# Kernel tuning notes

Measured on AMD Instinct MI355X. Metric: run time of the kernel, lower is better.

Reference implementation:

```python
import jax, jax.numpy as jnp
import numpy as np

N = 100000
E = 400000
G = 2000  # number of graphs in batch
IN_DIM = 32
H = 192
L = 4
EPS = 1e-5


def setup_inputs() -> dict:
    key = jax.random.key(0)
    ks = jax.random.split(key, 20)
    x = jax.random.normal(ks[0], (N, IN_DIM), jnp.float32)
    edge_src = jax.random.randint(ks[1], (E,), 0, N, jnp.int32)
    edge_dst = jax.random.randint(ks[2], (E,), 0, N, jnp.int32)
    batch = jnp.sort(jax.random.randint(ks[3], (N,), 0, G, jnp.int32))
    s_in = 1.0 / np.sqrt(IN_DIM)
    s_h = 1.0 / np.sqrt(H)
    return {
        "x": x,
        "edge_src": edge_src,
        "edge_dst": edge_dst,
        "batch": batch,
        # layer 0 (in_dim -> H); weights stored [in, out]
        "Wrel0": jax.random.uniform(ks[4], (IN_DIM, H), jnp.float32, -s_in, s_in),
        "brel0": jax.random.uniform(ks[5], (H,), jnp.float32, -s_in, s_in),
        "Wroot0": jax.random.uniform(ks[6], (IN_DIM, H), jnp.float32, -s_in, s_in),
        # layers 1..3 stacked (H -> H)
        "Wrel": jax.random.uniform(ks[7], (L - 1, H, H), jnp.float32, -s_h, s_h),
        "brel": jax.random.uniform(ks[8], (L - 1, H), jnp.float32, -s_h, s_h),
        "Wroot": jax.random.uniform(ks[9], (L - 1, H, H), jnp.float32, -s_h, s_h),
        # batchnorm affine params for all 4 layers
        "gamma": jnp.ones((L, H), jnp.float32),
        "beta": jnp.zeros((L, H), jnp.float32),
        # head MLP and output
        "Wh1": jax.random.uniform(ks[10], (H, H), jnp.float32, -s_h, s_h),
        "bh1": jax.random.uniform(ks[11], (H,), jnp.float32, -s_h, s_h),
        "Wh2": jax.random.uniform(ks[12], (H, H), jnp.float32, -s_h, s_h),
        "bh2": jax.random.uniform(ks[13], (H,), jnp.float32, -s_h, s_h),
        "Wout": jax.random.uniform(ks[14], (H, 1), jnp.float32, -s_h, s_h),
        "bout": jax.random.uniform(ks[15], (1,), jnp.float32, -s_h, s_h),
    }


def _rel_conv(x, edge_src, edge_dst, Wrel, brel, Wroot):
    # message: lin_rel(x_j); applying the linear at node level first is the
    # same math as per-edge (linear commutes with gather) and cheaper.
    h = x @ Wrel + brel                      # [N, out]
    agg = jax.ops.segment_sum(h[edge_src], edge_dst, num_segments=N)
    return agg + x @ Wroot


def _bn_relu(h, g, b):
    # BatchNorm1d in training mode: batch stats over node dim, biased var
    mu = h.mean(axis=0)
    var = jnp.var(h, axis=0)
    h = (h - mu) * jax.lax.rsqrt(var + EPS) * g + b
    return jax.nn.relu(h)


def reference(x, edge_src, edge_dst, batch, Wrel0, brel0, Wroot0,
              Wrel, brel, Wroot, gamma, beta, Wh1, bh1, Wh2, bh2, Wout, bout):
    h = _bn_relu(_rel_conv(x, edge_src, edge_dst, Wrel0, brel0, Wroot0),
                 gamma[0], beta[0])
    for i in range(L - 1):
        h = _bn_relu(_rel_conv(h, edge_src, edge_dst, Wrel[i], brel[i], Wroot[i]),
                     gamma[i + 1], beta[i + 1])
    # global mean pool over graphs
    sums = jax.ops.segment_sum(h, batch, num_segments=G)          # [G, H]
    cnt = jax.ops.segment_sum(jnp.ones((N,), h.dtype), batch, num_segments=G)
    g = sums / jnp.maximum(cnt, 1.0)[:, None]
    # head MLP (dropout is identity at eval) + output linear
    g = jax.nn.relu(g @ Wh1 + bh1) @ Wh2 + bh2
    return g @ Wout + bout                                        # [G, 1]
```

## Files before the change

### kernel.cpp

```cpp
#include <hip/hip_runtime.h>

#define HDIM 192
#define EPS 1e-5f

typedef __attribute__((ext_vector_type(8))) _Float16 half8;
typedef __attribute__((ext_vector_type(4))) float floatx4;

__device__ __forceinline__ float h2f(ushort u) {
    union { ushort u; _Float16 h; } c; c.u = u; return (float)c.h;
}
__device__ __forceinline__ ushort f2h(float x) {
    _Float16 h = (_Float16)x;
    union { _Float16 h; ushort u; } c; c.h = h; return c.u;
}
__device__ __forceinline__ uint4 pack8(const ushort* h) {
    uint4 p;
    p.x = h[0] | ((uint)h[1] << 16); p.y = h[2] | ((uint)h[3] << 16);
    p.z = h[4] | ((uint)h[5] << 16); p.w = h[6] | ((uint)h[7] << 16);
    return p;
}

__device__ __forceinline__ void gload_lds16(const ushort* g, ushort* l) {
    __builtin_amdgcn_global_load_lds(
        (const __attribute__((address_space(1))) unsigned int*)g,
        (__attribute__((address_space(3))) unsigned int*)l, 16, 0, 0);
}

#define WAITV0() asm volatile("s_waitcnt vmcnt(0)" ::: "memory")


struct PrepArgs {
    const float* src[6];
    ushort*      dst[6];
    int K[6];
    int off[7];
};

__global__ __launch_bounds__(256) void prep_all_k(PrepArgs a)
{
    int idx = blockIdx.x * 256 + threadIdx.x;
    if (idx >= a.off[6]) return;
    int i = 0;
    #pragma unroll
    for (int t = 1; t < 6; ++t) if (idx >= a.off[t]) i = t;
    int r = idx - a.off[i];
    int K = a.K[i];
    int perMat = (K >> 5) * 12 * 64;
    int mat = r / perMat;
    r -= mat * perMat;
    int lane = r & 63;
    int ct = (r >> 6) % 12;
    int kc = r / (12 * 64);
    int col = ct * 16 + (lane & 15);
    int kb  = kc * 32 + (lane >> 4) * 8;
    const float* Wm = a.src[i] + (size_t)mat * K * HDIM;
    ushort* base = a.dst[i] + (size_t)mat * K * HDIM;
    size_t o = (size_t)kc * 6144 + (size_t)(ct * 64 + lane) * 8;
    #pragma unroll
    for (int j = 0; j < 8; ++j)
        base[o + j] = f2h(Wm[(size_t)(kb + j) * HDIM + col]);
}

__global__ __launch_bounds__(256) void conv_half_k(
    const float* __restrict__ src, ushort* __restrict__ dst, int R, int C)
{
    int OC = C >> 3;
    int idx = blockIdx.x * 256 + threadIdx.x;
    if (idx >= R * OC) return;
    int r = idx / OC;
    int o = idx - r * OC;
    float4 v0 = ((const float4*)(src + (size_t)r * C + o * 8))[0];
    float4 v1 = ((const float4*)(src + (size_t)r * C + o * 8))[1];
    float v[8] = {v0.x, v0.y, v0.z, v0.w, v1.x, v1.y, v1.z, v1.w};
    ushort h[8];
    #pragma unroll
    for (int t = 0; t < 8; ++t) h[t] = f2h(v[t]);
    *(uint4*)(dst + (size_t)r * C + o * 8) = pack8(h);
}

template<bool DUAL, bool RELU, bool DEG, bool STATS, int NKC>
__global__ __launch_bounds__(256, 3) void gemm_mfma_k(
    const ushort* __restrict__ A1h, const ushort* __restrict__ W1f,
    const ushort* __restrict__ A2h, const ushort* __restrict__ W2f,
    const float* __restrict__ degf, const float* __restrict__ bias,
    ushort* __restrict__ C, float* __restrict__ pstats, int N, int K)
{
    constexpr int KR   = NKC * 32;
    constexpr int RS   = KR + 8;
    constexpr int SLAB = 64 * RS;
    constexpr int NINSTR = SLAB / 512;
    constexpr int NCH  = DUAL ? 2 * NKC : NKC;
    constexpr int SMEMU = ((DUAL ? 2 * SLAB : SLAB) > 12800)
                            ? (DUAL ? 2 * SLAB : SLAB) : 12800;

    __shared__ float sstat[2][HDIM];
    __shared__ __align__(16) ushort smem[SMEMU];
    const int tid  = threadIdx.x;
    const int wave = tid >> 6;
    const int lane = tid & 63;
    const int row0 = blockIdx.x * 64;
    const int m16 = lane & 15;
    const int g4  = lane >> 4;

    if (STATS && tid < HDIM) { sstat[0][tid] = 0.f; sstat[1][tid] = 0.f; }

    auto stage = [&](const ushort* Ab, int slabOff) {
        #pragma unroll
        for (int i = wave; i < NINSTR; i += 4) {
            int slotB = i * 1024 + lane * 16;
            int r   = slotB / (RS * 2);
            int off = slotB - r * (RS * 2);
            if (off >= KR * 2) off = KR * 2 - 16;
            int rr = row0 + r; if (rr >= N) rr = N - 1;
            gload_lds16(Ab + (size_t)rr * KR + (off >> 1),
                        smem + slabOff + i * 512);
        }
    };

    stage(A1h, 0);
    if constexpr (DUAL) stage(A2h, SLAB);
    WAITV0();
    __builtin_amdgcn_s_barrier();
    __builtin_amdgcn_sched_barrier(0);

    auto loadB = [&](int c, half8* b) {
        bool ph = DUAL && (c >= NKC);
        int kc = ph ? c - NKC : c;
        const ushort* Bp = (ph ? W2f : W1f) + (size_t)kc * 6144
                         + (size_t)(wave * 192 + lane) * 8;
        #pragma unroll
        for (int ct = 0; ct < 3; ++ct)
            b[ct] = *(const half8*)(Bp + ct * 512);
    };

    floatx4 acc[4][3];
    #pragma unroll
    for (int s = 0; s < 4; ++s)
        #pragma unroll
        for (int ct = 0; ct < 3; ++ct) acc[s][ct] = (floatx4){0.f, 0.f, 0.f, 0.f};

    half8 bA[3], bB[3];
    loadB(0, bA);
    #pragma unroll
    for (int c = 0; c < NCH; ++c) {
        if (c + 1 < NCH) loadB(c + 1, (c & 1) ? bA : bB);
        const int base = (DUAL && c >= NKC) ? SLAB : 0;
        const int kc   = (DUAL && c >= NKC) ? c - NKC : c;
        const ushort* aB = smem + base + m16 * RS + kc * 32 + g4 * 8;
        half8 a[4];
        #pragma unroll
        for (int s = 0; s < 4; ++s)
            a[s] = *(const half8*)(aB + s * 16 * RS);
        const half8* bu = (c & 1) ? bB : bA;
        #pragma unroll
        for (int ct = 0; ct < 3; ++ct)
            #pragma unroll
            for (int s = 0; s < 4; ++s)
                acc[s][ct] = __builtin_amdgcn_mfma_f32_16x16x32_f16(a[s], bu[ct], acc[s][ct], 0, 0, 0);
    }

    __syncthreads();
    #pragma unroll
    for (int ct = 0; ct < 3; ++ct) {
        int col = wave * 48 + ct * 16 + m16;
        float bv = bias ? bias[col] : 0.f;
        float lsum = 0.f, lsq = 0.f;
        #pragma unroll
        for (int s = 0; s < 4; ++s) {
            #pragma unroll
            for (int reg = 0; reg < 4; ++reg) {
                int rloc = s * 16 + g4 * 4 + reg;
                int rr = row0 + rloc;
                int rrc = rr < N ? rr : N - 1;
                float v = acc[s][ct][reg] + (DEG ? degf[rrc] * bv : bv);
                if (STATS && rr < N) { lsum += v; lsq += v * v; }
                if (RELU) v = fmaxf(v, 0.f);
                smem[rloc * 200 + col] = f2h(v);
            }
        }
        if (STATS) {
            lsum += __shfl_xor(lsum, 16); lsum += __shfl_xor(lsum, 32);
            lsq  += __shfl_xor(lsq, 16);  lsq  += __shfl_xor(lsq, 32);
            if (g4 == 0) {
                atomicAdd(&sstat[0][col], lsum);
                atomicAdd(&sstat[1][col], lsq);
            }
        }
    }
    __syncthreads();
    {
        int rowsLeft = N - row0; if (rowsLeft > 64) rowsLeft = 64;
        int lim = rowsLeft * 24;
        ushort* Cb = C + (size_t)row0 * HDIM;
        #pragma unroll
        for (int k = 0; k < 6; ++k) {
            int u = tid + k * 256;
            if (u < lim) {
                int r  = u / 24;
                int c8 = (u - r * 24) * 8;
                *(uint4*)(Cb + (size_t)u * 8) =
                    *(const uint4*)(smem + r * 200 + c8);
            }
        }
    }
    if (STATS) {
        if (tid < HDIM) {
            float* pb = pstats + (size_t)blockIdx.x * (2 * HDIM);
            pb[tid]        = sstat[0][tid];
            pb[HDIM + tid] = sstat[1][tid];
        }
    }
}

__global__ __launch_bounds__(256, 3) void gemm_fused_k(
    const ushort* __restrict__ Hraw, const ushort* __restrict__ W1f,
    const ushort* __restrict__ W2f,
    const float* __restrict__ degf, const float* __restrict__ bias,
    const float* __restrict__ instats, const float* __restrict__ gammaL,
    const float* __restrict__ betaL, float invN,
    const int* __restrict__ row_ptr, const int* __restrict__ col,
    ushort* __restrict__ C, float* __restrict__ pstats, int N)
{
    constexpr int KR   = 192;
    constexpr int RS   = 200;
    constexpr int SLAB = 64 * RS;
    constexpr int NINSTR = SLAB / 512;
    constexpr int NKC  = 6, NCH = 12;

    __shared__ float sstat[2][HDIM];
    __shared__ __align__(16) ushort smem[2 * SLAB];
    const int tid  = threadIdx.x;
    const int wave = tid >> 6;
    const int lane = tid & 63;
    const int row0 = blockIdx.x * 64;
    const int m16 = lane & 15;
    const int g4  = lane >> 4;

    #pragma unroll
    for (int i = wave; i < NINSTR; i += 4) {
        int slotB = i * 1024 + lane * 16;
        int r   = slotB / (RS * 2);
        int off = slotB - r * (RS * 2);
        if (off >= KR * 2) off = KR * 2 - 16;
        int rr = row0 + r; if (rr >= N) rr = N - 1;
        gload_lds16(Hraw + (size_t)rr * KR + (off >> 1),
                    smem + SLAB + i * 512);
    }
    WAITV0();
    __builtin_amdgcn_s_barrier();
    __builtin_amdgcn_sched_barrier(0);

    if (tid < HDIM) {
        float mu  = instats[tid] * invN;
        float var = instats[HDIM + tid] * invN - mu * mu;
        float s = gammaL[tid] * rsqrtf(var + EPS);
        sstat[0][tid] = s;
        sstat[1][tid] = betaL[tid] - mu * s;
    }
    __syncthreads();

    const int r = tid >> 2, q = tid & 3;
    {
        ushort* rowp = smem + SLAB + r * RS + q * 48;
        #pragma unroll
        for (int k = 0; k < 6; ++k) {
            uint4 hv = *(uint4*)(rowp + k * 8);
            uint hu[4] = {hv.x, hv.y, hv.z, hv.w};
            ushort oh[8];
            #pragma unroll
            for (int e = 0; e < 4; ++e) {
                int ch = q * 48 + k * 8 + e * 2;
                float v0 = h2f((ushort)(hu[e] & 0xffffu)) * sstat[0][ch]     + sstat[1][ch];
                float v1 = h2f((ushort)(hu[e] >> 16))     * sstat[0][ch + 1] + sstat[1][ch + 1];
                oh[2*e]   = f2h(fmaxf(v0, 0.f));
                oh[2*e+1] = f2h(fmaxf(v1, 0.f));
            }
            *(uint4*)(rowp + k * 8) = pack8(oh);
        }
    }
    {
        float acc[48];
        #pragma unroll
        for (int i = 0; i < 48; ++i) acc[i] = 0.f;
        int rr = row0 + r;
        if (rr < N) {
            int j0 = row_ptr[rr], j1 = row_ptr[rr + 1];
            const ushort* hp = Hraw + q * 48;
            for (int j = j0; j < j1; ++j) {
                int s = col[j];
                const ushort* rp = hp + (size_t)s * KR;
                #pragma unroll
                for (int ck = 0; ck < 6; ++ck) {
                    uint4 hv = *(const uint4*)(rp + ck * 8);
                    uint hu[4] = {hv.x, hv.y, hv.z, hv.w};
                    #pragma unroll
                    for (int e = 0; e < 4; ++e) {
                        int ch = q * 48 + ck * 8 + e * 2;
                        float v0 = h2f((ushort)(hu[e] & 0xffffu)) * sstat[0][ch]     + sstat[1][ch];
                        float v1 = h2f((ushort)(hu[e] >> 16))     * sstat[0][ch + 1] + sstat[1][ch + 1];
                        acc[ck*8 + e*2]     += fmaxf(v0, 0.f);
                        acc[ck*8 + e*2 + 1] += fmaxf(v1, 0.f);
                    }
                }
            }
        }
        ushort* dst = smem + r * RS + q * 48;
        #pragma unroll
        for (int ck = 0; ck < 6; ++ck) {
            ushort oh[8];
            #pragma unroll
            for (int e = 0; e < 8; ++e) oh[e] = f2h(acc[ck*8 + e]);
            *(uint4*)(dst + ck * 8) = pack8(oh);
        }
    }
    __syncthreads();
    if (tid < HDIM) { sstat[0][tid] = 0.f; sstat[1][tid] = 0.f; }

    auto loadB = [&](int c, half8* b) {
        bool ph = (c >= NKC);
        int kc = ph ? c - NKC : c;
        const ushort* Bp = (ph ? W2f : W1f) + (size_t)kc * 6144
                         + (size_t)(wave * 192 + lane) * 8;
        #pragma unroll
        for (int ct = 0; ct < 3; ++ct)
            b[ct] = *(const half8*)(Bp + ct * 512);
    };

    floatx4 acc[4][3];
    #pragma unroll
    for (int s = 0; s < 4; ++s)
        #pragma unroll
        for (int ct = 0; ct < 3; ++ct) acc[s][ct] = (floatx4){0.f, 0.f, 0.f, 0.f};

    half8 bA[3], bB[3];
    loadB(0, bA);
    #pragma unroll
    for (int c = 0; c < NCH; ++c) {
        if (c + 1 < NCH) loadB(c + 1, (c & 1) ? bA : bB);
        const int base = (c >= NKC) ? SLAB : 0;
        const int kc   = (c >= NKC) ? c - NKC : c;
        const ushort* aB = smem + base + m16 * RS + kc * 32 + g4 * 8;
        half8 a[4];
        #pragma unroll
        for (int s = 0; s < 4; ++s)
            a[s] = *(const half8*)(aB + s * 16 * RS);
        const half8* bu = (c & 1) ? bB : bA;
        #pragma unroll
        for (int ct = 0; ct < 3; ++ct)
            #pragma unroll
            for (int s = 0; s < 4; ++s)
                acc[s][ct] = __builtin_amdgcn_mfma_f32_16x16x32_f16(a[s], bu[ct], acc[s][ct], 0, 0, 0);
    }

    __syncthreads();
    #pragma unroll
    for (int ct = 0; ct < 3; ++ct) {
        int colc = wave * 48 + ct * 16 + m16;
        float bv = bias[colc];
        float lsum = 0.f, lsq = 0.f;
        #pragma unroll
        for (int s = 0; s < 4; ++s) {
            #pragma unroll
            for (int reg = 0; reg < 4; ++reg) {
                int rloc = s * 16 + g4 * 4 + reg;
                int rr = row0 + rloc;
                int rrc = rr < N ? rr : N - 1;
                float v = acc[s][ct][reg] + degf[rrc] * bv;
                if (rr < N) { lsum += v; lsq += v * v; }
                smem[rloc * 200 + colc] = f2h(v);
            }
        }
        lsum += __shfl_xor(lsum, 16); lsum += __shfl_xor(lsum, 32);
        lsq  += __shfl_xor(lsq, 16);  lsq  += __shfl_xor(lsq, 32);
        if (g4 == 0) {
            atomicAdd(&sstat[0][colc], lsum);
            atomicAdd(&sstat[1][colc], lsq);
        }
    }
    __syncthreads();
    {
        int rowsLeft = N - row0; if (rowsLeft > 64) rowsLeft = 64;
        int lim = rowsLeft * 24;
        ushort* Cb = C + (size_t)row0 * HDIM;
        #pragma unroll
        for (int k = 0; k < 6; ++k) {
            int u = tid + k * 256;
            if (u < lim) {
                int rr = u / 24;
                int c8 = (u - rr * 24) * 8;
                *(uint4*)(Cb + (size_t)u * 8) =
                    *(const uint4*)(smem + rr * 200 + c8);
            }
        }
    }
    if (tid < HDIM) {
        float* pb = pstats + (size_t)blockIdx.x * (2 * HDIM);
        pb[tid]        = sstat[0][tid];
        pb[HDIM + tid] = sstat[1][tid];
    }
}

__global__ __launch_bounds__(256) void bn_reduce_k(
    const float* __restrict__ pbuf, float* __restrict__ stats, int nb)
{
    __shared__ float red[32][9];
    int t  = threadIdx.x;
    int cl = t & 7;
    int s  = t >> 3;
    int c  = blockIdx.x * 8 + cl;
    float acc = 0.f;
    int b = s;
    for (; b + 96 < nb; b += 128) {
        float a0 = pbuf[(size_t)b * 384 + c];
        float a1 = pbuf[(size_t)(b + 32) * 384 + c];
        float a2 = pbuf[(size_t)(b + 64) * 384 + c];
        float a3 = pbuf[(size_t)(b + 96) * 384 + c];
        acc += a0 + a1 + a2 + a3;
    }
    for (; b < nb; b += 32)
        acc += pbuf[(size_t)b * 384 + c];
    red[s][cl] = acc;
    __syncthreads();
    if (t < 8) {
        float a = 0.f;
        #pragma unroll
        for (int i = 0; i < 32; ++i) a += red[i][t];
        stats[blockIdx.x * 8 + t] = a;
    }
}

__global__ __launch_bounds__(256) void hist_k(
    const int* __restrict__ dst, int* __restrict__ deg, int E)
{
    int e = blockIdx.x * 256 + threadIdx.x;
    if (e < E) atomicAdd(&deg[dst[e]], 1);
}

__global__ __launch_bounds__(256) void block_sum_k(
    const int* __restrict__ deg, int* __restrict__ bsum, int N)
{
    __shared__ int s[256];
    int t = threadIdx.x;
    int n = blockIdx.x * 256 + t;
    s[t] = (n < N) ? deg[n] : 0;
    __syncthreads();
    for (int off = 128; off > 0; off >>= 1) {
        if (t < off) s[t] += s[t + off];
        __syncthreads();
    }
    if (t == 0) bsum[blockIdx.x] = s[0];
}

__global__ __launch_bounds__(512) void scan_bsum_k(int* __restrict__ bsum, int nb)
{
    __shared__ int s[512];
    int t = threadIdx.x;
    int v = (t < nb) ? bsum[t] : 0;
    s[t] = v;
    __syncthreads();
    for (int off = 1; off < 512; off <<= 1) {
        int u = (t >= off) ? s[t - off] : 0;
        __syncthreads();
        s[t] += u;
        __syncthreads();
    }
    if (t < nb) bsum[t] = s[t] - v;
}

__global__ __launch_bounds__(256) void row_ptr_k(
    const int* __restrict__ deg, const int* __restrict__ bsum,
    int* __restrict__ row_ptr, int* __restrict__ cursor,
    float* __restrict__ degf, int N, int E)
{
    __shared__ int s[256];
    int t = threadIdx.x;
    int n = blockIdx.x * 256 + t;
    int v = (n < N) ? deg[n] : 0;
    s[t] = v;
    __syncthreads();
    for (int off = 1; off < 256; off <<= 1) {
        int u = (t >= off) ? s[t - off] : 0;
        __syncthreads();
        s[t] += u;
        __syncthreads();
    }
    int ex = s[t] - v + bsum[blockIdx.x];
    if (n < N) {
        row_ptr[n] = ex;
        cursor[n]  = ex;
        degf[n]    = (float)v;
    }
    if (blockIdx.x == 0 && t == 0) row_ptr[N] = E;
}

__global__ __launch_bounds__(256) void fill_k(
    const int* __restrict__ src, const int* __restrict__ dst,
    int* __restrict__ cursor, int* __restrict__ col, int E)
{
    int e = blockIdx.x * 256 + threadIdx.x;
    if (e < E) {
        int p = atomicAdd(&cursor[dst[e]], 1);
        col[p] = src[e];
    }
}

__global__ __launch_bounds__(256) void gather_h_k(
    const ushort* __restrict__ xh, const int* __restrict__ row_ptr,
    const int* __restrict__ col, ushort* __restrict__ gh, int N, int K)
{
    int OC = K >> 3;
    int idx = blockIdx.x * 256 + threadIdx.x;
    if (idx >= N * OC) return;
    int n = idx / OC;
    int o = idx - n * OC;
    const ushort* hp = xh + o * 8;
    int j0 = row_ptr[n], j1 = row_ptr[n + 1];
    float acc[8] = {0.f,0.f,0.f,0.f,0.f,0.f,0.f,0.f};
    auto addrow = [&](uint4 hv) {
        uint hu[4] = {hv.x, hv.y, hv.z, hv.w};
        #pragma unroll
        for (int t = 0; t < 4; ++t) {
            acc[2*t]   += h2f((ushort)(hu[t] & 0xffffu));
            acc[2*t+1] += h2f((ushort)(hu[t] >> 16));
        }
    };
    int j = j0;
    for (; j + 3 < j1; j += 4) {
        int s0 = col[j], s1 = col[j+1], s2 = col[j+2], s3 = col[j+3];
        uint4 v0 = *(const uint4*)(hp + (size_t)s0 * K);
        uint4 v1 = *(const uint4*)(hp + (size_t)s1 * K);
        uint4 v2 = *(const uint4*)(hp + (size_t)s2 * K);
        uint4 v3 = *(const uint4*)(hp + (size_t)s3 * K);
        addrow(v0); addrow(v1); addrow(v2); addrow(v3);
    }
    for (; j < j1; ++j)
        addrow(*(const uint4*)(hp + (size_t)col[j] * K));
    ushort oh[8];
    #pragma unroll
    for (int t = 0; t < 8; ++t) oh[t] = f2h(acc[t]);
    *(uint4*)(gh + (size_t)n * K + o * 8) = pack8(oh);
}

__global__ __launch_bounds__(192) void pool_bn_k(
    const ushort* __restrict__ h, const float* __restrict__ stats,
    const float* __restrict__ gamma, const float* __restrict__ beta,
    float invN, const int* __restrict__ batch,
    ushort* __restrict__ gsh, int G, int N)
{
    __shared__ int bounds[2];
    int g = blockIdx.x;
    int c = threadIdx.x;
    if (c < 2) {
        int key = g + c;
        int lo = 0, hi = N;
        while (lo < hi) {
            int mid = (lo + hi) >> 1;
            if (batch[mid] < key) lo = mid + 1; else hi = mid;
        }
        bounds[c] = lo;
    }
    __syncthreads();
    int r0 = bounds[0], r1 = bounds[1];
    float mu  = stats[c] * invN;
    float var = stats[HDIM + c] * invN - mu * mu;
    float sc  = gamma[c] * rsqrtf(var + EPS);
    float sh  = beta[c] - mu * sc;
    const ushort* base = h + c;
    float s = 0.f;
    for (int r = r0; r < r1; ++r)
        s += fmaxf(h2f(base[(size_t)r * HDIM]) * sc + sh, 0.f);
    float m = s / fmaxf((float)(r1 - r0), 1.f);
    gsh[(size_t)g * HDIM + c] = f2h(m);
}

__global__ __launch_bounds__(64) void out_dot_k(
    const ushort* __restrict__ g2h, const float* __restrict__ Wout,
    const float* __restrict__ bout, float* __restrict__ out, int G)
{
    int gi = blockIdx.x;
    int t = threadIdx.x;
    float s = 0.f;
    #pragma unroll
    for (int j = 0; j < 3; ++j) {
        int c = t + j * 64;
        s += h2f(g2h[(size_t)gi * HDIM + c]) * Wout[c];
    }
    #pragma unroll
    for (int off = 32; off > 0; off >>= 1) s += __shfl_down(s, off, 64);
    if (t == 0) out[gi] = s + bout[0];
}

extern "C" void kernel_launch(void* const* d_in, const int* in_sizes, int n_in,
                              void* d_out, int out_size, void* d_ws, size_t ws_size,
                              hipStream_t stream)
{
    const float* x      = (const float*)d_in[0];
    const int*   esrc   = (const int*)d_in[1];
    const int*   edst   = (const int*)d_in[2];
    const int*   batch  = (const int*)d_in[3];
    const float* Wrel0  = (const float*)d_in[4];
    const float* brel0  = (const float*)d_in[5];
    const float* Wroot0 = (const float*)d_in[6];
    const float* Wrel   = (const float*)d_in[7];
    const float* brel   = (const float*)d_in[8];
    const float* Wroot  = (const float*)d_in[9];
    const float* gamma  = (const float*)d_in[10];
    const float* beta   = (const float*)d_in[11];
    const float* Wh1    = (const float*)d_in[12];
    const float* bh1    = (const float*)d_in[13];
    const float* Wh2    = (const float*)d_in[14];
    const float* bh2    = (const float*)d_in[15];
    const float* Wout   = (const float*)d_in[16];
    const float* bout   = (const float*)d_in[17];
    float* out = (float*)d_out;

    const int N  = in_sizes[3];
    const int E  = in_sizes[1];
    const int K0 = in_sizes[0] / N;
    const int G  = out_size;
    const int nBlocks = (N + 255) / 256;
    const float invN = 1.0f / (float)N;

    char* p = (char*)d_ws;
    auto carve = [&](size_t bytes) -> void* {
        void* r = (void*)p; p += (bytes + 255) & ~(size_t)255; return r;
    };
    ushort* bufa_h= (ushort*)carve((size_t)N * HDIM * 2);
    ushort* bufb_h= (ushort*)carve((size_t)N * HDIM * 2);
    ushort* xh    = (ushort*)carve((size_t)N * K0 * 2);
    ushort* gh    = (ushort*)carve((size_t)N * K0 * 2);
    ushort* gsh   = (ushort*)carve((size_t)G * HDIM * 2);
    ushort* g1h   = (ushort*)carve((size_t)G * HDIM * 2);
    ushort* g2h   = (ushort*)carve((size_t)G * HDIM * 2);
    int*    deg   = (int*)   carve((size_t)N * 4);
    float*  bnsums= (float*) carve(4 * 2 * HDIM * 4);
    size_t  zspan = (char*)(bnsums + 4 * 2 * HDIM) - (char*)deg;
    float*  degf  = (float*) carve((size_t)N * 4);
    int*    row_ptr=(int*)   carve((size_t)(N + 1) * 4);
    int*    cursor= (int*)   carve((size_t)N * 4);
    int*    col   = (int*)   carve((size_t)E * 4);
    int*    bsum  = (int*)   carve((size_t)nBlocks * 4);
    ushort* Wrel0f= (ushort*)carve((size_t)K0 * HDIM * 2);
    ushort* Wroot0f=(ushort*)carve((size_t)K0 * HDIM * 2);
    ushort* Wrelf = (ushort*)carve((size_t)3 * HDIM * HDIM * 2);
    ushort* Wrootf= (ushort*)carve((size_t)3 * HDIM * HDIM * 2);
    ushort* Wh1f  = (ushort*)carve((size_t)HDIM * HDIM * 2);
    ushort* Wh2f  = (ushort*)carve((size_t)HDIM * HDIM * 2);

    dim3 b256(256);
    const int eBlocks = (E + 255) / 256;
    const int gemmN = (N + 63) / 64;
    const int gemmG = (G + 63) / 64;

    float*  pbuf  = (float*) carve((size_t)gemmN * 2 * HDIM * 4);

    {
        PrepArgs a;
        int t0 = (K0 >> 5) * 12 * 64;
        int t1 = (HDIM >> 5) * 12 * 64;
        a.src[0] = Wrel0;  a.dst[0] = Wrel0f;  a.K[0] = K0;
        a.src[1] = Wroot0; a.dst[1] = Wroot0f; a.K[1] = K0;
        a.src[2] = Wrel;   a.dst[2] = Wrelf;   a.K[2] = HDIM;
        a.src[3] = Wroot;  a.dst[3] = Wrootf;  a.K[3] = HDIM;
        a.src[4] = Wh1;    a.dst[4] = Wh1f;    a.K[4] = HDIM;
        a.src[5] = Wh2;    a.dst[5] = Wh2f;    a.K[5] = HDIM;
        a.off[0] = 0;
        a.off[1] = a.off[0] + t0;
        a.off[2] = a.off[1] + t0;
        a.off[3] = a.off[2] + 3 * t1;
        a.off[4] = a.off[3] + 3 * t1;
        a.off[5] = a.off[4] + t1;
        a.off[6] = a.off[5] + t1;
        prep_all_k<<<(a.off[6] + 255) / 256, b256, 0, stream>>>(a);
    }
    conv_half_k<<<((N * (K0 >> 3)) + 255) / 256, b256, 0, stream>>>(x, xh, N, K0);

    hipMemsetAsync(deg, 0, zspan, stream);
    hist_k<<<eBlocks, b256, 0, stream>>>(edst, deg, E);
    block_sum_k<<<nBlocks, b256, 0, stream>>>(deg, bsum, N);
    scan_bsum_k<<<1, dim3(512), 0, stream>>>(bsum, nBlocks);
    row_ptr_k<<<nBlocks, b256, 0, stream>>>(deg, bsum, row_ptr, cursor, degf, N, E);
    fill_k<<<eBlocks, b256, 0, stream>>>(esrc, edst, cursor, col, E);

    gather_h_k<<<((N * (K0 >> 3)) + 255) / 256, b256, 0, stream>>>(
        xh, row_ptr, col, gh, N, K0);
    gemm_mfma_k<true, false, true, true, 1><<<gemmN, b256, 0, stream>>>(
        gh, Wrel0f, xh, Wroot0f, degf, brel0, bufa_h, pbuf, N, K0);
    bn_reduce_k<<<48, b256, 0, stream>>>(pbuf, bnsums, gemmN);

    ushort* rd = bufa_h;
    ushort* wr = bufb_h;
    for (int l = 1; l < 4; ++l) {
        const ushort* Wrf = Wrelf  + (size_t)(l - 1) * HDIM * HDIM;
        const ushort* Wtf = Wrootf + (size_t)(l - 1) * HDIM * HDIM;
        const float*  br  = brel   + (size_t)(l - 1) * HDIM;
        const float*  st  = bnsums + (size_t)(l - 1) * 2 * HDIM;
        const float*  gm  = gamma  + (size_t)(l - 1) * HDIM;
        const float*  bt  = beta   + (size_t)(l - 1) * HDIM;
        gemm_fused_k<<<gemmN, b256, 0, stream>>>(
            rd, Wrf, Wtf, degf, br, st, gm, bt, invN,
            row_ptr, col, wr, pbuf, N);
        bn_reduce_k<<<48, b256, 0, stream>>>(pbuf, bnsums + l * 2 * HDIM, gemmN);
        ushort* tmp = rd; rd = wr; wr = tmp;
    }

    pool_bn_k<<<G, dim3(192), 0, stream>>>(
        rd, bnsums + 3 * 2 * HDIM, gamma + 3 * HDIM, beta + 3 * HDIM,
        invN, batch, gsh, G, N);

    gemm_mfma_k<false, true, false, false, 6><<<gemmG, b256, 0, stream>>>(
        gsh, Wh1f, nullptr, nullptr, nullptr, bh1, g1h, nullptr, G, HDIM);
    gemm_mfma_k<false, false, false, false, 6><<<gemmG, b256, 0, stream>>>(
        g1h, Wh2f, nullptr, nullptr, nullptr, bh2, g2h, nullptr, G, HDIM);
    out_dot_k<<<G, dim3(64), 0, stream>>>(g2h, Wout, bout, out, G);
}
```

Measured before the change: 474.3 us.

## Use 512 threads per block in fused gather-GEMM kernel with 8 threads per row

New measurement: 447.4 us. 1.06x faster.

```diff
diff --git a/kernel.cpp b/kernel.cpp
--- a/kernel.cpp
+++ b/kernel.cpp
@@ -212,7 +212,7 @@
     }
 }
 
-__global__ __launch_bounds__(256, 3) void gemm_fused_k(
+__global__ __launch_bounds__(512, 4) void gemm_fused_k(
     const ushort* __restrict__ Hraw, const ushort* __restrict__ W1f,
     const ushort* __restrict__ W2f,
     const float* __restrict__ degf, const float* __restrict__ bias,
@@ -237,7 +237,7 @@
     const int g4  = lane >> 4;
 
     #pragma unroll
-    for (int i = wave; i < NINSTR; i += 4) {
+    for (int i = wave; i < NINSTR; i += 8) {
         int slotB = i * 1024 + lane * 16;
         int r   = slotB / (RS * 2);
         int off = slotB - r * (RS * 2);
@@ -259,17 +259,18 @@
     }
     __syncthreads();
 
-    const int r = tid >> 2, q = tid & 3;
+    const int r  = tid >> 3;
+    const int q8 = tid & 7;
     {
-        ushort* rowp = smem + SLAB + r * RS + q * 48;
-        #pragma unroll
-        for (int k = 0; k < 6; ++k) {
+        ushort* rowp = smem + SLAB + r * RS + q8 * 24;
+        #pragma unroll
+        for (int k = 0; k < 3; ++k) {
             uint4 hv = *(uint4*)(rowp + k * 8);
             uint hu[4] = {hv.x, hv.y, hv.z, hv.w};
             ushort oh[8];
             #pragma unroll
             for (int e = 0; e < 4; ++e) {
-                int ch = q * 48 + k * 8 + e * 2;
+                int ch = q8 * 24 + k * 8 + e * 2;
                 float v0 = h2f((ushort)(hu[e] & 0xffffu)) * sstat[0][ch]     + sstat[1][ch];
                 float v1 = h2f((ushort)(hu[e] >> 16))     * sstat[0][ch + 1] + sstat[1][ch + 1];
                 oh[2*e]   = f2h(fmaxf(v0, 0.f));
@@ -279,34 +280,34 @@
         }
     }
     {
-        float acc[48];
-        #pragma unroll
-        for (int i = 0; i < 48; ++i) acc[i] = 0.f;
+        float acc[24];
+        #pragma unroll
+        for (int i = 0; i < 24; ++i) acc[i] = 0.f;
         int rr = row0 + r;
         if (rr < N) {
             int j0 = row_ptr[rr], j1 = row_ptr[rr + 1];
-            const ushort* hp = Hraw + q * 48;
+            const ushort* hp = Hraw + q8 * 24;
             for (int j = j0; j < j1; ++j) {
                 int s = col[j];
                 const ushort* rp = hp + (size_t)s * KR;
+                uint4 h0 = *(const uint4*)(rp);
+                uint4 h1 = *(const uint4*)(rp + 8);
+                uint4 h2 = *(const uint4*)(rp + 16);
+                uint hu[12] = {h0.x,h0.y,h0.z,h0.w, h1.x,h1.y,h1.z,h1.w,
+                               h2.x,h2.y,h2.z,h2.w};
                 #pragma unroll
-                for (int ck = 0; ck < 6; ++ck) {
-                    uint4 hv = *(const uint4*)(rp + ck * 8);
-                    uint hu[4] = {hv.x, hv.y, hv.z, hv.w};
-                    #pragma unroll
-                    for (int e = 0; e < 4; ++e) {
-                        int ch = q * 48 + ck * 8 + e * 2;
-                        float v0 = h2f((ushort)(hu[e] & 0xffffu)) * sstat[0][ch]     + sstat[1][ch];
-                        float v1 = h2f((ushort)(hu[e] >> 16))     * sstat[0][ch + 1] + sstat[1][ch + 1];
-                        acc[ck*8 + e*2]     += fmaxf(v0, 0.f);
-                        acc[ck*8 + e*2 + 1] += fmaxf(v1, 0.f);
-                    }
+                for (int e = 0; e < 12; ++e) {
+                    int ch = q8 * 24 + e * 2;
+                    float v0 = h2f((ushort)(hu[e] & 0xffffu)) * sstat[0][ch]     + sstat[1][ch];
+                    float v1 = h2f((ushort)(hu[e] >> 16))     * sstat[0][ch + 1] + sstat[1][ch + 1];
+                    acc[e*2]     += fmaxf(v0, 0.f);
+                    acc[e*2 + 1] += fmaxf(v1, 0.f);
                 }
             }
         }
-        ushort* dst = smem + r * RS + q * 48;
-        #pragma unroll
-        for (int ck = 0; ck < 6; ++ck) {
+        ushort* dst = smem + r * RS + q8 * 24;
+        #pragma unroll
+        for (int ck = 0; ck < 3; ++ck) {
             ushort oh[8];
             #pragma unroll
             for (int e = 0; e < 8; ++e) oh[e] = f2h(acc[ck*8 + e]);
@@ -316,19 +317,22 @@
     __syncthreads();
     if (tid < HDIM) { sstat[0][tid] = 0.f; sstat[1][tid] = 0.f; }
 
+    const int rg = wave >> 2;
+    const int cg = wave & 3;
+
     auto loadB = [&](int c, half8* b) {
         bool ph = (c >= NKC);
         int kc = ph ? c - NKC : c;
         const ushort* Bp = (ph ? W2f : W1f) + (size_t)kc * 6144
-                         + (size_t)(wave * 192 + lane) * 8;
+                         + (size_t)(cg * 192 + lane) * 8;
         #pragma unroll
         for (int ct = 0; ct < 3; ++ct)
             b[ct] = *(const half8*)(Bp + ct * 512);
     };
 
-    floatx4 acc[4][3];
-    #pragma unroll
-    for (int s = 0; s < 4; ++s)
+    floatx4 acc[2][3];
+    #pragma unroll
+    for (int s = 0; s < 2; ++s)
         #pragma unroll
         for (int ct = 0; ct < 3; ++ct) acc[s][ct] = (floatx4){0.f, 0.f, 0.f, 0.f};
 
@@ -339,30 +343,30 @@
         if (c + 1 < NCH) loadB(c + 1, (c & 1) ? bA : bB);
         const int base = (c >= NKC) ? SLAB : 0;
         const int kc   = (c >= NKC) ? c - NKC : c;
-        const ushort* aB = smem + base + m16 * RS + kc * 32 + g4 * 8;
-        half8 a[4];
-        #pragma unroll
-        for (int s = 0; s < 4; ++s)
+        const ushort* aB = smem + base + (rg * 32 + m16) * RS + kc * 32 + g4 * 8;
+        half8 a[2];
+        #pragma unroll
+        for (int s = 0; s < 2; ++s)
             a[s] = *(const half8*)(aB + s * 16 * RS);
         const half8* bu = (c & 1) ? bB : bA;
         #pragma unroll
         for (int ct = 0; ct < 3; ++ct)
             #pragma unroll
-            for (int s = 0; s < 4; ++s)
+            for (int s = 0; s < 2; ++s)
                 acc[s][ct] = __builtin_amdgcn_mfma_f32_16x16x32_f16(a[s], bu[ct], acc[s][ct], 0, 0, 0);
     }
 
     __syncthreads();
     #pragma unroll
     for (int ct = 0; ct < 3; ++ct) {
-        int colc = wave * 48 + ct * 16 + m16;
+        int colc = cg * 48 + ct * 16 + m16;
         float bv = bias[colc];
         float lsum = 0.f, lsq = 0.f;
         #pragma unroll
-        for (int s = 0; s < 4; ++s) {
+        for (int s = 0; s < 2; ++s) {
             #pragma unroll
             for (int reg = 0; reg < 4; ++reg) {
-                int rloc = s * 16 + g4 * 4 + reg;
+                int rloc = rg * 32 + s * 16 + g4 * 4 + reg;
                 int rr = row0 + rloc;
                 int rrc = rr < N ? rr : N - 1;
                 float v = acc[s][ct][reg] + degf[rrc] * bv;
@@ -383,8 +387,8 @@
         int lim = rowsLeft * 24;
         ushort* Cb = C + (size_t)row0 * HDIM;
         #pragma unroll
-        for (int k = 0; k < 6; ++k) {
-            int u = tid + k * 256;
+        for (int k = 0; k < 3; ++k) {
+            int u = tid + k * 512;
             if (u < lim) {
                 int rr = u / 24;
                 int c8 = (u - rr * 24) * 8;
@@ -697,7 +701,7 @@
         const float*  st  = bnsums + (size_t)(l - 1) * 2 * HDIM;
         const float*  gm  = gamma  + (size_t)(l - 1) * HDIM;
         const float*  bt  = beta   + (size_t)(l - 1) * HDIM;
-        gemm_fused_k<<<gemmN, b256, 0, stream>>>(
+        gemm_fused_k<<<gemmN, dim3(512), 0, stream>>>(
             rd, Wrf, Wtf, degf, br, st, gm, bt, invN,
             row_ptr, col, wr, pbuf, N);
         bn_reduce_k<<<48, b256, 0, stream>>>(pbuf, bnsums + l * 2 * HDIM, gemmN);
```
